# Kernel optimization log

Measured on AMD Instinct MI355X. Metric: run time of the kernel, lower is better.

Reference implementation:

```python
import jax, jax.numpy as jnp
import numpy as np

N, K, M, DIN, DOUT = 4096, 16, 65536, 256, 256


def setup_inputs() -> dict:
    key = jax.random.key(0)
    ks = jax.random.split(key, 16)
    s = 1.0 / np.sqrt(DOUT)
    x = jax.random.normal(ks[0], (N, DIN), jnp.float32)
    h_tensor = jax.random.normal(ks[1], (M, DOUT), jnp.float32)
    c_tensor = jax.random.normal(ks[2], (M, DOUT), jnp.float32)
    # variable-length child lists: lengths in [1, K], -1 padding like get_nums()
    lengths = jax.random.randint(ks[3], (N,), 1, K + 1)
    idx = jax.random.randint(ks[4], (N, K), 0, M)
    t = jnp.arange(K)[None, :]
    indice = jnp.where(t < lengths[:, None], idx, -1).astype(jnp.int32)
    W_w = jax.random.normal(ks[5], (4 * DOUT, DIN), jnp.float32) * s
    W_b = jax.random.normal(ks[6], (4 * DOUT,), jnp.float32) * s
    h0 = jax.random.normal(ks[7], (4, DOUT), jnp.float32)
    c0 = jax.random.normal(ks[8], (4, DOUT), jnp.float32)
    Wih = jax.random.normal(ks[9], (4, 2, 4 * DOUT, DOUT), jnp.float32) * s
    Whh = jax.random.normal(ks[10], (4, 2, 4 * DOUT, DOUT), jnp.float32) * s
    bih = jax.random.normal(ks[11], (4, 2, 4 * DOUT), jnp.float32) * s
    bhh = jax.random.normal(ks[12], (4, 2, 4 * DOUT), jnp.float32) * s
    fc = jax.random.normal(ks[13], (4, DOUT, 2 * DOUT), jnp.float32) * s
    return dict(x=x, h_tensor=h_tensor, c_tensor=c_tensor, indice=indice,
                W_w=W_w, W_b=W_b, h0=h0, c0=c0, Wih=Wih, Whh=Whh,
                bih=bih, bhh=bhh, fc=fc)


def _lstm_dir(xseq, mask, h_init, c_init, W_ih, W_hh, b, reverse):
    """Masked LSTM over child axis. xseq [N,K,d], mask [N,K] bool. Mimics
    pack_padded_sequence: state frozen and output 0 at padded steps."""
    d = h_init.shape[-1]
    xs = jnp.swapaxes(xseq, 0, 1)   # [K,N,d]
    ms = jnp.swapaxes(mask, 0, 1)   # [K,N]

    def step(carry, inp):
        h, c = carry
        xt, mt = inp
        g = xt @ W_ih.T + h @ W_hh.T + b        # [N,4d], gate order i,f,g,o
        i = jax.nn.sigmoid(g[:, :d])
        f = jax.nn.sigmoid(g[:, d:2 * d])
        u = jnp.tanh(g[:, 2 * d:3 * d])
        o = jax.nn.sigmoid(g[:, 3 * d:])
        c_new = f * c + i * u
        h_new = o * jnp.tanh(c_new)
        m = mt[:, None]
        return (jnp.where(m, h_new, h), jnp.where(m, c_new, c)), jnp.where(m, h_new, 0.0)

    _, ys = jax.lax.scan(step, (h_init, c_init), (xs, ms), reverse=reverse)
    return jnp.swapaxes(ys, 0, 1)   # [N,K,d]


def _bilstm_seq(xseq, mask, h0j, c0j, Wihj, Whhj, bihj, bhhj, fcj):
    n = xseq.shape[0]
    h_init = jnp.broadcast_to(h0j, (n, h0j.shape[-1]))
    c_init = jnp.broadcast_to(c0j, (n, c0j.shape[-1]))
    yf = _lstm_dir(xseq, mask, h_init, c_init, Wihj[0], Whhj[0], bihj[0] + bhhj[0], False)
    yb = _lstm_dir(xseq, mask, h_init, c_init, Wihj[1], Whhj[1], bihj[1] + bhhj[1], True)
    y = jnp.concatenate([yf, yb], axis=-1)      # [N,K,2d]
    return jnp.einsum('nkh,dh->nkd', y, fcj)    # fc (no bias); 0 stays 0 at pads


def reference(x, h_tensor, c_tensor, indice, W_w, W_b, h0, c0, Wih, Whh, bih, bhh, fc):
    mask = indice != -1                           # [N,K]
    length = mask.sum(axis=1)                     # [N], >= 1
    safe_idx = jnp.where(mask, indice, 0)
    h = h_tensor[safe_idx]                        # [N,K,d] gather of child states
    c = c_tensor[safe_idx]
    Wx = x @ W_w.T + W_b                          # [N,4d]
    d = DOUT
    Wf, Wi, Wu, Wo = Wx[:, :d], Wx[:, d:2 * d], Wx[:, 2 * d:3 * d], Wx[:, 3 * d:]
    ys = [_bilstm_seq(h, mask, h0[j], c0[j], Wih[j], Whh[j], bih[j], bhh[j], fc[j])
          for j in range(4)]                      # U_f, U_i, U_u, U_o
    # forget branch: per-child gate, masked sum over children
    branch_f_k = jax.nn.sigmoid(Wf[:, None, :] + ys[0])
    branch_f = jnp.sum(branch_f_k * c * mask[..., None], axis=1)
    # i/u/o use last valid timestep (packed LSTM y_last)
    ar = jnp.arange(x.shape[0])
    last = length - 1
    branch_i = jax.nn.sigmoid(ys[1][ar, last] + Wi)
    branch_u = jnp.tanh(ys[2][ar, last] + Wu)
    branch_o = jax.nn.sigmoid(ys[3][ar, last] + Wo)
    new_c = branch_i * branch_u + branch_f
    new_h = branch_o * jnp.tanh(new_c)
    return new_h, new_c
```

## Files before the change

kernel.cpp:

```cpp
#include <hip/hip_runtime.h>
#include <math.h>

#define N_SEQ 4096
#define KCH   16
#define DM    256
#define G4    1024
#define LP    40
#define EP    68

typedef __attribute__((ext_vector_type(8))) short bf8;
typedef __attribute__((ext_vector_type(4))) float f4;

__device__ __forceinline__ float fast_rcp(float x) { return __builtin_amdgcn_rcpf(x); }
__device__ __forceinline__ float sigf(float x)   { return fast_rcp(1.f + __expf(-x)); }
__device__ __forceinline__ float tanh_f(float x) { return 1.f - 2.f * fast_rcp(1.f + __expf(2.f * x)); }

__device__ __forceinline__ float bf2f(unsigned short u) {
    return __uint_as_float(((unsigned)u) << 16);
}
__device__ __forceinline__ unsigned short f2bf(float f) {
    unsigned u = __float_as_uint(f);
    unsigned r = (u + 0x7fffu + ((u >> 16) & 1u)) >> 16;
    return (unsigned short)r;
}
__device__ __forceinline__ unsigned pack2(float a, float b) {
    return (unsigned)f2bf(a) | ((unsigned)f2bf(b) << 16);
}

#define GLDS(gp, lp) __builtin_amdgcn_global_load_lds( \
    (const __attribute__((address_space(1))) void*)(gp), \
    (__attribute__((address_space(3))) void*)(lp), 16, 0, 0)

#define VW(n) asm volatile("s_waitcnt vmcnt(" #n ")" ::: "memory")

template<int NSEG, int LDB>
__device__ __forceinline__ void pass_pipe(
    const unsigned short* const (&segA)[NSEG],
    const unsigned short* const (&segB)[NSEG],
    unsigned short* SM,
    f4 (&acc)[4][4], int wave, int wm, int wn, int jq, int fr)
{
    constexpr int NS = NSEG * 8;
    constexpr int L  = 4;
    constexpr int NP = (NS < L) ? NS : L;

#pragma unroll
    for (int p = 0; p < NP; ++p) {
        const unsigned short* A_ = segA[p >> 3] + (p & 7) * 32;
        const unsigned short* B_ = segB[p >> 3] + (p & 7) * 32;
        unsigned short* a = SM + (p % 5) * 8192 + wave * 1024;
        unsigned short* b = a + 4096;
        GLDS(A_, a);        GLDS(A_ + 16 * DM, a + 512);
        GLDS(B_, b);        GLDS(B_ + 16 * LDB, b + 512);
    }
#pragma unroll
    for (int t = 0; t < NS; ++t) {
        const int rem = NS - 1 - t;
        if (rem >= 3)      VW(12);
        else if (rem == 2) VW(8);
        else if (rem == 1) VW(4);
        else               VW(0);
        __builtin_amdgcn_s_barrier();

        if (t + L < NS) {
            const int tn = t + L;
            const unsigned short* A_ = segA[tn >> 3] + (tn & 7) * 32;
            const unsigned short* B_ = segB[tn >> 3] + (tn & 7) * 32;
            unsigned short* a = SM + (tn % 5) * 8192 + wave * 1024;
            unsigned short* b = a + 4096;
            GLDS(A_, a);    GLDS(A_ + 16 * DM, a + 512);
            GLDS(B_, b);    GLDS(B_ + 16 * LDB, b + 512);
        }

        const unsigned short* Ab = SM + (t % 5) * 8192;
        const unsigned short* Bb = Ab + 4096;
        bf8 af[4], bb[4];
#pragma unroll
        for (int i = 0; i < 4; ++i)
            af[i] = *(const bf8*)(Ab + (wm + i * 16 + fr) * 32 + jq);
#pragma unroll
        for (int j = 0; j < 4; ++j)
            bb[j] = *(const bf8*)(Bb + (wn + j * 16 + fr) * 32 + jq);

        __builtin_amdgcn_s_setprio(1);
#pragma unroll
        for (int i = 0; i < 4; ++i)
#pragma unroll
            for (int j = 0; j < 4; ++j)
                acc[i][j] = __builtin_amdgcn_mfma_f32_16x16x32_bf16(
                    af[i], bb[j], acc[i][j], 0, 0, 0);
        __builtin_amdgcn_s_setprio(0);
    }
}

template<int KLEN>
__device__ __forceinline__ void pass_bf(
    const unsigned short* __restrict__ aRow,
    const unsigned short* __restrict__ bRow,
    unsigned short* Asm, unsigned short* Bsm, f4 (&acc)[4][4])
{
    const int tid  = threadIdx.x;
    const int kh   = (tid & 1) * 16;
    const int srow = tid >> 1;
    const int lane = tid & 63, wave = tid >> 6;
    const int wm = (wave >> 1) * 64, wn = (wave & 1) * 64;
    const int fr = lane & 15, fk = (lane >> 4) * 8;
    unsigned short* da = Asm + srow * LP + kh;
    unsigned short* db = Bsm + srow * LP + kh;

    for (int k0 = 0; k0 < KLEN; k0 += 32) {
        __syncthreads();
        *(int4*)(da)     = *(const int4*)(aRow + k0 + kh);
        *(int4*)(da + 8) = *(const int4*)(aRow + k0 + kh + 8);
        *(int4*)(db)     = *(const int4*)(bRow + k0 + kh);
        *(int4*)(db + 8) = *(const int4*)(bRow + k0 + kh + 8);
        __syncthreads();
        bf8 af[4], bb[4];
#pragma unroll
        for (int i = 0; i < 4; ++i)
            af[i] = *(const bf8*)(Asm + (wm + i * 16 + fr) * LP + fk);
#pragma unroll
        for (int j = 0; j < 4; ++j)
            bb[j] = *(const bf8*)(Bsm + (wn + j * 16 + fr) * LP + fk);
#pragma unroll
        for (int i = 0; i < 4; ++i)
#pragma unroll
            for (int j = 0; j < 4; ++j)
                acc[i][j] = __builtin_amdgcn_mfma_f32_16x16x32_bf16(
                    af[i], bb[j], acc[i][j], 0, 0, 0);
    }
}

template<int KLEN>
__device__ __forceinline__ void pass_f32(
    const float* __restrict__ aRow,
    const unsigned short* __restrict__ bRow,
    unsigned short* Asm, unsigned short* Bsm, f4 (&acc)[4][4])
{
    const int tid  = threadIdx.x;
    const int kh   = (tid & 1) * 16;
    const int srow = tid >> 1;
    const int lane = tid & 63, wave = tid >> 6;
    const int wm = (wave >> 1) * 64, wn = (wave & 1) * 64;
    const int fr = lane & 15, fk = (lane >> 4) * 8;
    unsigned short* da = Asm + srow * LP + kh;
    unsigned short* db = Bsm + srow * LP + kh;

    for (int k0 = 0; k0 < KLEN; k0 += 32) {
        __syncthreads();
        {
            const float* s = aRow + k0 + kh;
            float4 v0 = *(const float4*)(s);
            float4 v1 = *(const float4*)(s + 4);
            float4 v2 = *(const float4*)(s + 8);
            float4 v3 = *(const float4*)(s + 12);
            *(int4*)(da)     = make_int4(pack2(v0.x, v0.y), pack2(v0.z, v0.w),
                                         pack2(v1.x, v1.y), pack2(v1.z, v1.w));
            *(int4*)(da + 8) = make_int4(pack2(v2.x, v2.y), pack2(v2.z, v2.w),
                                         pack2(v3.x, v3.y), pack2(v3.z, v3.w));
        }
        *(int4*)(db)     = *(const int4*)(bRow + k0 + kh);
        *(int4*)(db + 8) = *(const int4*)(bRow + k0 + kh + 8);
        __syncthreads();
        bf8 af[4], bb[4];
#pragma unroll
        for (int i = 0; i < 4; ++i)
            af[i] = *(const bf8*)(Asm + (wm + i * 16 + fr) * LP + fk);
#pragma unroll
        for (int j = 0; j < 4; ++j)
            bb[j] = *(const bf8*)(Bsm + (wn + j * 16 + fr) * LP + fk);
#pragma unroll
        for (int i = 0; i < 4; ++i)
#pragma unroll
            for (int j = 0; j < 4; ++j)
                acc[i][j] = __builtin_amdgcn_mfma_f32_16x16x32_bf16(
                    af[i], bb[j], acc[i][j], 0, 0, 0);
    }
}


__global__ __launch_bounds__(256) void k_lastidx(
    const int* __restrict__ indice, int* __restrict__ last_idx)
{
    const int n = blockIdx.x * 256 + threadIdx.x;
    if (n >= N_SEQ) return;
    int len = 0;
#pragma unroll
    for (int k = 0; k < KCH; ++k) len += (indice[n * KCH + k] != -1);
    last_idx[n] = indice[n * KCH + (len - 1)];
}

__global__ __launch_bounds__(1024) void k_hh0_bsum2(
    const float* __restrict__ bih, const float* __restrict__ bhh,
    const float* __restrict__ h0, const float* __restrict__ Whh,
    float* __restrict__ bsum2)
{
    const int jz = blockIdx.x, j = jz + 1;
    const int g = threadIdx.x;
    const int jd = j * 2 + 1;
    const float* wrow = Whh + ((size_t)jd * G4 + g) * DM;
    float s = bih[jd * G4 + g] + bhh[jd * G4 + g];
    for (int h = 0; h < DM; ++h) s = fmaf(h0[j * DM + h], wrow[h], s);
    const int c = (g & 255) * 4 + (g >> 8);
    bsum2[jz * G4 + c] = s;
}

__global__ __launch_bounds__(256) void k_init_states(
    const float* __restrict__ h0, const float* __restrict__ c0,
    unsigned short* __restrict__ hA, float* __restrict__ c_state)
{
    const int row = blockIdx.x;
    const int s = row >> 12;
    const int tree = (s < 4) ? s : 0;
    const int d = threadIdx.x;
    hA[(size_t)row * DM + d]      = f2bf(h0[tree * DM + d]);
    c_state[(size_t)row * DM + d] = c0[tree * DM + d];
}

__global__ __launch_bounds__(256) void k_zero4(float4* __restrict__ p)
{
    p[(size_t)blockIdx.x * 256 + threadIdx.x] = make_float4(0.f, 0.f, 0.f, 0.f);
}

__global__ __launch_bounds__(256) void k_prep_wcat(
    const float* __restrict__ Wih, const float* __restrict__ Whh,
    const float* __restrict__ bih, const float* __restrict__ bhh,
    unsigned short* __restrict__ wcat, float* __restrict__ bsumr)
{
    const int c = blockIdx.x, s = blockIdx.y;
    const int wsel = (s < 4) ? s * 2 : 1;
    const int d = c >> 2, g = c & 3;
    const size_t srcrow = ((size_t)wsel * G4 + g * DM + d) * DM;
    unsigned short* dst = wcat + ((size_t)s * G4 + c) * 512;
    const int t = threadIdx.x;
    dst[t]       = f2bf(Wih[srcrow + t]);
    dst[256 + t] = f2bf(Whh[srcrow + t]);
    if (t == 0)
        bsumr[s * G4 + c] = bih[wsel * G4 + g * DM + d] + bhh[wsel * G4 + g * DM + d];
}

__global__ __launch_bounds__(256) void k_prep_wcat2(
    const float* __restrict__ Wih, unsigned short* __restrict__ wcat2)
{
    const int c = blockIdx.x, jz = blockIdx.y, j = jz + 1;
    const int d = c >> 2, g = c & 3;
    const size_t srcrow = ((size_t)(j * 2 + 1) * G4 + g * DM + d) * DM;
    wcat2[((size_t)jz * G4 + c) * 256 + threadIdx.x] = f2bf(Wih[srcrow + threadIdx.x]);
}

__global__ __launch_bounds__(256) void k_prep_fcb(
    const float* __restrict__ fc, unsigned short* __restrict__ fcb)
{
    const int dout = blockIdx.x, z = blockIdx.y, t = threadIdx.x;
    fcb[((size_t)z * DM + dout) * DM + t] = f2bf(fc[(size_t)dout * 512 + z * DM + t]);
}

__global__ __launch_bounds__(256) void k_prep_fcb2(
    const float* __restrict__ fc, unsigned short* __restrict__ fcb2)
{
    const int dout = blockIdx.x, jz = blockIdx.y, j = jz + 1, t = threadIdx.x;
    const float* src = fc + ((size_t)j * DM + dout) * 512;
    unsigned short* dst = fcb2 + ((size_t)jz * DM + dout) * 512;
    dst[t]       = f2bf(src[t]);
    dst[t + 256] = f2bf(src[t + 256]);
}

__global__ __launch_bounds__(256) void k_prep_wwb(
    const float* __restrict__ W_w, unsigned short* __restrict__ wwb)
{
    const size_t i = (size_t)blockIdx.x * 256 + threadIdx.x;
    wwb[i] = f2bf(W_w[i]);
}

__device__ __forceinline__ void gather_slice(
    const float* __restrict__ h_tensor, const int* __restrict__ indice,
    unsigned short* __restrict__ xbuf, int zz, int kk, int blk)
{
    const int row = blk * 64 + (threadIdx.x >> 2);
    const int cb  = (threadIdx.x & 3) * 64;
    int idx = indice[row * KCH + kk]; if (idx < 0) idx = 0;
    const float* src = h_tensor + (size_t)idx * DM + cb;
    unsigned short* dst = xbuf + ((size_t)zz * N_SEQ + row) * DM + cb;
#pragma unroll
    for (int c = 0; c < 64; c += 4) {
        float4 v = *(const float4*)(src + c);
        *(uint2*)(dst + c) = make_uint2(pack2(v.x, v.y), pack2(v.z, v.w));
    }
}

__global__ __launch_bounds__(256) void k_gather_x0(
    const float* __restrict__ h_tensor, const int* __restrict__ indice,
    unsigned short* __restrict__ xbuf)
{
    const int slice = blockIdx.x >> 6, blk = blockIdx.x & 63;
    gather_slice(h_tensor, indice, xbuf, slice, slice ? (KCH - 1) : 0, blk);
}

__global__ __launch_bounds__(256) void k_scan_merged(
    const unsigned short* __restrict__ xb_cur, unsigned short* __restrict__ xb_nxt,
    const unsigned short* __restrict__ yb_prev, unsigned short* __restrict__ yb_cur,
    const int* __restrict__ indice, const float* __restrict__ h_tensor,
    const unsigned short* __restrict__ h_in, unsigned short* __restrict__ h_out,
    float* __restrict__ c_state,
    const unsigned short* __restrict__ wcat, const float* __restrict__ bsumr,
    const unsigned short* __restrict__ fcb, unsigned short* __restrict__ ys0,
    int r)
{
    __shared__ __align__(16) unsigned short SMEM[40960];

    const int tid  = threadIdx.x;
    const int lane = tid & 63, wave = tid >> 6;
    const int wm = (wave >> 1) * 64, wn = (wave & 1) * 64;
    const int fr = lane & 15;
    const int jq = ((lane >> 4) ^ ((fr >> 1) & 3)) * 8;
    const int lr = wave * 32 + (lane >> 2);
    const int jl = ((lane & 3) ^ ((lane >> 3) & 3)) * 8;

    const int bz = blockIdx.z;

    if (bz == 5) {
        const int id5 = blockIdx.x + 8 * blockIdx.y;
        if (id5 >= 128) {
            const int rr = r + 1;
            if (rr >= KCH) return;
            const int g = id5 - 128;
            const int zz = g >> 6;
            gather_slice(h_tensor, indice, xb_nxt, zz,
                         zz ? (KCH - 1 - rr) : rr, g & 63);
            return;
        }
        if (r == 0) return;
        const int rp = r - 1;
        const int z = id5 >> 6;
        const int kslice = z ? (KCH - 1 - rp) : rp;
        const int row0 = (id5 & 31) * 128;
        const int c0 = ((id5 >> 5) & 1) * 128;

        const unsigned short* ay0 = yb_prev + ((size_t)z * N_SEQ + row0 + lr) * DM + jl;
        const unsigned short* bf0 = fcb + ((size_t)z * DM + c0 + lr) * DM + jl;

        f4 acc[4][4];
#pragma unroll
        for (int i = 0; i < 4; ++i)
#pragma unroll
            for (int j = 0; j < 4; ++j) acc[i][j] = (f4)(0.f);
        {
            const unsigned short* const segA[1] = { ay0 };
            const unsigned short* const segB[1] = { bf0 };
            pass_pipe<1, 256>(segA, segB, SMEM, acc, wave, wm, wn, jq, fr);
        }

#pragma unroll
        for (int i = 0; i < 4; ++i)
#pragma unroll
            for (int j = 0; j < 4; ++j) {
                const int col = c0 + wn + j * 16 + fr;
#pragma unroll
                for (int reg = 0; reg < 4; ++reg) {
                    const int rowg = row0 + wm + i * 16 + (lane >> 4) * 4 + reg;
                    const size_t ix = ((size_t)rowg * KCH + kslice) * DM + col;
                    ys0[ix] = f2bf(bf2f(ys0[ix]) + acc[i][j][reg]);
                }
            }
        return;
    }

    const int s = bz;
    const int k = (s < 4) ? r : (KCH - 1 - r);
    const int z = (s < 4) ? 0 : 1;
    const int bn = blockIdx.y & 7;
    const int bm = (blockIdx.y >> 3) * 8 + blockIdx.x;
    const int row0 = bm * 128, c0 = bn * 128;

    const unsigned short* xz = xb_cur + (size_t)z * N_SEQ * DM;
    const unsigned short* hs_in = h_in + (size_t)s * N_SEQ * DM;
    const unsigned short* ax0 = xz + (size_t)(row0 + lr) * DM + jl;
    const unsigned short* ah0 = hs_in + (size_t)(row0 + lr) * DM + jl;
    const unsigned short* bw0 = wcat + ((size_t)s * G4 + c0 + lr) * 512 + jl;

    f4 acc[4][4];
#pragma unroll
    for (int i = 0; i < 4; ++i)
#pragma unroll
        for (int j = 0; j < 4; ++j) acc[i][j] = (f4)(0.f);

    {
        const unsigned short* const segA[2] = { ax0, ah0 };
        const unsigned short* const segB[2] = { bw0, bw0 + 256 };
        pass_pipe<2, 512>(segA, segB, SMEM, acc, wave, wm, wn, jq, fr);
    }

    float* sc = (float*)SMEM + wave * (16 * EP);
    __syncthreads();
    const int kprev = (s < 4) ? (k - 1) : (k + 1);
#pragma unroll
    for (int i = 0; i < 4; ++i) {
#pragma unroll
        for (int j = 0; j < 4; ++j) {
            const int colL = j * 16 + fr;
            const int rbase = (lane >> 4) * 4;
#pragma unroll
            for (int reg = 0; reg < 4; ++reg)
                sc[(rbase + reg) * EP + colL] = acc[i][j][reg];
        }
        asm volatile("s_waitcnt lgkmcnt(0)" ::: "memory");
        __builtin_amdgcn_sched_barrier(0);
        const int rowg = row0 + wm + i * 16 + fr;
        const bool m = (indice[rowg * KCH + k] != -1);
        const bool mpv = (r == 0) ? true : (indice[rowg * KCH + kprev] != -1);
#pragma unroll
        for (int q = 0; q < 4; ++q) {
            const int dL = (lane >> 4) + q * 4;
            const f4 gv = *(const f4*)(sc + fr * EP + dL * 4);
            const f4 bb = *(const f4*)(bsumr + s * G4 + c0 + wn + dL * 4);
            const int d = ((c0 + wn) >> 2) + dL;
            const size_t cix = ((size_t)s * N_SEQ + rowg) * DM + d;
            unsigned short hv = 0;
            if (m) {
                const float ii = sigf(gv.x + bb.x);
                const float ff = sigf(gv.y + bb.y);
                const float uu = tanh_f(gv.z + bb.z);
                const float oo = sigf(gv.w + bb.w);
                const float c_old = c_state[cix];
                const float cn = ff * c_old + ii * uu;
                c_state[cix] = cn;
                hv = f2bf(oo * tanh_f(cn));
                h_out[cix] = hv;
            } else if (mpv) {
                h_out[cix] = hs_in[(size_t)rowg * DM + d];
            }
            if (s == 0)
                yb_cur[(size_t)rowg * DM + d] = m ? hv : (unsigned short)0;
            else if (s == 4)
                yb_cur[(size_t)(N_SEQ + rowg) * DM + d] = m ? hv : (unsigned short)0;
        }
        asm volatile("s_waitcnt lgkmcnt(0)" ::: "memory");
        __builtin_amdgcn_sched_barrier(0);
    }
}

__global__ __launch_bounds__(256) void k_acc_tail(
    const unsigned short* __restrict__ ybuf, const unsigned short* __restrict__ fcb,
    unsigned short* __restrict__ ys0)
{
    __shared__ __align__(16) unsigned short SMEM[40960];
    const int tid = threadIdx.x;
    const int lane = tid & 63, wave = tid >> 6;
    const int wm = (wave >> 1) * 64, wn = (wave & 1) * 64;
    const int fr = lane & 15;
    const int jq = ((lane >> 4) ^ ((fr >> 1) & 3)) * 8;
    const int lr = wave * 32 + (lane >> 2);
    const int jl = ((lane & 3) ^ ((lane >> 3) & 3)) * 8;

    const int z = blockIdx.z;
    const int kslice = z ? 0 : (KCH - 1);
    const int row0 = blockIdx.y * 128, c0 = blockIdx.x * 128;

    const unsigned short* ay0 = ybuf + ((size_t)z * N_SEQ + row0 + lr) * DM + jl;
    const unsigned short* bf0 = fcb + ((size_t)z * DM + c0 + lr) * DM + jl;

    f4 acc[4][4];
#pragma unroll
    for (int i = 0; i < 4; ++i)
#pragma unroll
        for (int j = 0; j < 4; ++j) acc[i][j] = (f4)(0.f);
    {
        const unsigned short* const segA[1] = { ay0 };
        const unsigned short* const segB[1] = { bf0 };
        pass_pipe<1, 256>(segA, segB, SMEM, acc, wave, wm, wn, jq, fr);
    }

#pragma unroll
    for (int i = 0; i < 4; ++i)
#pragma unroll
        for (int j = 0; j < 4; ++j) {
            const int col = c0 + wn + j * 16 + fr;
#pragma unroll
            for (int reg = 0; reg < 4; ++reg) {
                const int rowg = row0 + wm + i * 16 + (lane >> 4) * 4 + reg;
                const size_t ix = ((size_t)rowg * KCH + kslice) * DM + col;
                ys0[ix] = f2bf(bf2f(ys0[ix]) + acc[i][j][reg]);
            }
        }
}


__global__ __launch_bounds__(256) void k_bwd_mfma(
    const float* __restrict__ h_tensor, const int* __restrict__ last_idx,
    const unsigned short* __restrict__ wcat2, const float* __restrict__ bsum2,
    const float* __restrict__ c0, unsigned short* __restrict__ yb_last)
{
    __shared__ __align__(16) unsigned short SMEM[2 * 128 * LP];
    const int jz = blockIdx.z, j = jz + 1;
    const int row0 = blockIdx.y * 128, c0t = blockIdx.x * 128;
    const int tid = threadIdx.x;
    const int srow = tid >> 1;

    const float* aF = h_tensor + (size_t)last_idx[row0 + srow] * DM;
    const unsigned short* bR = wcat2 + ((size_t)jz * G4 + c0t + srow) * 256;

    f4 acc[4][4];
#pragma unroll
    for (int i = 0; i < 4; ++i)
#pragma unroll
        for (int jj = 0; jj < 4; ++jj) acc[i][jj] = (f4)(0.f);

    pass_f32<256>(aF, bR, SMEM, SMEM + 128 * LP, acc);

    const int lane = tid & 63, wave = tid >> 6;
    const int wm = (wave >> 1) * 64, wn = (wave & 1) * 64;
    float* sc = (float*)SMEM + wave * (16 * EP);

    __syncthreads();
#pragma unroll
    for (int i = 0; i < 4; ++i) {
#pragma unroll
        for (int jj = 0; jj < 4; ++jj) {
            const int colL = jj * 16 + (lane & 15);
            const int rbase = (lane >> 4) * 4;
#pragma unroll
            for (int reg = 0; reg < 4; ++reg)
                sc[(rbase + reg) * EP + colL] = acc[i][jj][reg];
        }
        __syncthreads();
        const int rowg = row0 + wm + i * 16 + (lane & 15);
#pragma unroll
        for (int q = 0; q < 4; ++q) {
            const int dL = (lane >> 4) + q * 4;
            const f4 gv = *(const f4*)(sc + (lane & 15) * EP + dL * 4);
            const f4 bb = *(const f4*)(bsum2 + jz * G4 + c0t + wn + dL * 4);
            const int d = ((c0t + wn) >> 2) + dL;
            const float ii = sigf(gv.x + bb.x);
            const float ff = sigf(gv.y + bb.y);
            const float uu = tanh_f(gv.z + bb.z);
            const float oo = sigf(gv.w + bb.w);
            const float cn = ff * c0[j * DM + d] + ii * uu;
            yb_last[((size_t)jz * N_SEQ + rowg) * DM + d] = f2bf(oo * tanh_f(cn));
        }
        __syncthreads();
    }
}

__global__ __launch_bounds__(256) void k_wx_mfma(
    const float* __restrict__ x, const unsigned short* __restrict__ wwb,
    const float* __restrict__ W_b, unsigned short* __restrict__ Wx)
{
    __shared__ __align__(16) unsigned short SMEM[2 * 128 * LP];
    const int row0 = blockIdx.y * 128, c0 = blockIdx.x * 128;
    const int tid = threadIdx.x;
    const int srow = tid >> 1;

    const float* aF = x + (size_t)(row0 + srow) * DM;
    const unsigned short* bR = wwb + (size_t)(c0 + srow) * DM;

    f4 acc[4][4];
#pragma unroll
    for (int i = 0; i < 4; ++i)
#pragma unroll
        for (int j = 0; j < 4; ++j) acc[i][j] = (f4)(0.f);

    pass_f32<256>(aF, bR, SMEM, SMEM + 128 * LP, acc);

    const int lane = tid & 63, wave = tid >> 6;
    const int wm = (wave >> 1) * 64, wn = (wave & 1) * 64;
#pragma unroll
    for (int i = 0; i < 4; ++i)
#pragma unroll
        for (int j = 0; j < 4; ++j) {
            const int col = c0 + wn + j * 16 + (lane & 15);
            const float bv = W_b[col];
#pragma unroll
            for (int reg = 0; reg < 4; ++reg) {
                const int rowg = row0 + wm + i * 16 + (lane >> 4) * 4 + reg;
                Wx[(size_t)rowg * G4 + col] = f2bf(acc[i][j][reg] + bv);
            }
        }
}

__global__ __launch_bounds__(256) void k_fc_last_mfma(
    const unsigned short* __restrict__ h_final, const unsigned short* __restrict__ yb_last,
    const unsigned short* __restrict__ fcb2, unsigned short* __restrict__ ys_last)
{
    __shared__ __align__(16) unsigned short SMEM[2 * 128 * LP];
    const int jz = blockIdx.z;
    const int row0 = blockIdx.y * 128, c0 = blockIdx.x * 128;
    const int tid = threadIdx.x;
    const int srow = tid >> 1;

    const unsigned short* aH1 = h_final + ((size_t)(1 + jz) * N_SEQ + row0 + srow) * DM;
    const unsigned short* aH2 = yb_last + ((size_t)jz * N_SEQ + row0 + srow) * DM;
    const unsigned short* bR  = fcb2 + ((size_t)jz * DM + c0 + srow) * 512;

    f4 acc[4][4];
#pragma unroll
    for (int i = 0; i < 4; ++i)
#pragma unroll
        for (int j = 0; j < 4; ++j) acc[i][j] = (f4)(0.f);

    pass_bf<256>(aH1, bR, SMEM, SMEM + 128 * LP, acc);
    pass_bf<256>(aH2, bR + 256, SMEM, SMEM + 128 * LP, acc);

    const int lane = tid & 63, wave = tid >> 6;
    const int wm = (wave >> 1) * 64, wn = (wave & 1) * 64;
#pragma unroll
    for (int i = 0; i < 4; ++i)
#pragma unroll
        for (int j = 0; j < 4; ++j) {
            const int col = c0 + wn + j * 16 + (lane & 15);
#pragma unroll
            for (int reg = 0; reg < 4; ++reg) {
                const int rowg = row0 + wm + i * 16 + (lane >> 4) * 4 + reg;
                ys_last[((size_t)jz * N_SEQ + rowg) * DM + col] = f2bf(acc[i][j][reg]);
            }
        }
}

__global__ __launch_bounds__(256) void k_final(
    const unsigned short* __restrict__ Wx, const unsigned short* __restrict__ ys0,
    const unsigned short* __restrict__ ys_last, const float* __restrict__ c_tensor,
    const int* __restrict__ indice, float* __restrict__ out)
{
    const int n = blockIdx.x, d = threadIdx.x;
    const float Wf = bf2f(Wx[(size_t)n * G4 + d]);
    const float Wi = bf2f(Wx[(size_t)n * G4 + DM + d]);
    const float Wu = bf2f(Wx[(size_t)n * G4 + 2 * DM + d]);
    const float Wo = bf2f(Wx[(size_t)n * G4 + 3 * DM + d]);
    float bf = 0.f;
#pragma unroll
    for (int k = 0; k < KCH; ++k) {
        const int id = indice[n * KCH + k];
        if (id >= 0)
            bf += sigf(Wf + bf2f(ys0[((size_t)n * KCH + k) * DM + d])) *
                  c_tensor[(size_t)id * DM + d];
    }
    const float bi = sigf(bf2f(ys_last[((size_t)0 * N_SEQ + n) * DM + d]) + Wi);
    const float bu = tanh_f(bf2f(ys_last[((size_t)1 * N_SEQ + n) * DM + d]) + Wu);
    const float bo = sigf(bf2f(ys_last[((size_t)2 * N_SEQ + n) * DM + d]) + Wo);
    const float nc = bi * bu + bf;
    const float nh = bo * tanh_f(nc);
    out[(size_t)n * DM + d] = nh;
    out[(size_t)N_SEQ * DM + (size_t)n * DM + d] = nc;
}

extern "C" void kernel_launch(void* const* d_in, const int* in_sizes, int n_in,
                              void* d_out, int out_size, void* d_ws, size_t ws_size,
                              hipStream_t stream)
{
    const float* x        = (const float*)d_in[0];
    const float* h_tensor = (const float*)d_in[1];
    const float* c_tensor = (const float*)d_in[2];
    const int*   indice   = (const int*)d_in[3];
    const float* W_w      = (const float*)d_in[4];
    const float* W_b      = (const float*)d_in[5];
    const float* h0       = (const float*)d_in[6];
    const float* c0       = (const float*)d_in[7];
    const float* Wih      = (const float*)d_in[8];
    const float* Whh      = (const float*)d_in[9];
    const float* bih      = (const float*)d_in[10];
    const float* bhh      = (const float*)d_in[11];
    const float* fc       = (const float*)d_in[12];
    float* out = (float*)d_out;

    char* base = (char*)d_ws;
    float*          c_state  = (float*)(base + 0);
    int*            last_idx = (int*)  (base + 20971520);
    float*          bsumr    = (float*)(base + 20987904);
    unsigned short* hA       = (unsigned short*)(base + 21008384);
    unsigned short* hB       = (unsigned short*)(base + 31494144);
    unsigned short* ys0      = (unsigned short*)(base + 41979904);
    unsigned short* ybufA    = (unsigned short*)(base + 75534336);
    unsigned short* ybufB    = (unsigned short*)(base + 79728640);
    unsigned short* xbufA    = (unsigned short*)(base + 83922944);
    unsigned short* fcb      = (unsigned short*)(base + 88117248);
    unsigned short* postbuf  = (unsigned short*)(base + 88379392);
    unsigned short* wcat     = (unsigned short*)(base + 92573696);
    const size_t need = 97816576;
    if (ws_size < need) return;

    unsigned short* xbufB   = postbuf;
    unsigned short* wcat2   = postbuf;
    unsigned short* fcb2    = postbuf + 786432;
    unsigned short* wwb     = postbuf + 1179648;
    float*          bsum2   = (float*)(postbuf + 1441792);
    unsigned short* yb_last = ybufA;
    unsigned short* ys_last = hB;
    unsigned short* WxBuf   = hA;

    k_lastidx<<<16, 256, 0, stream>>>(indice, last_idx);
    k_init_states<<<5 * N_SEQ, 256, 0, stream>>>(h0, c0, hA, c_state);
    k_zero4<<<8192, 256, 0, stream>>>((float4*)ys0);
    k_prep_wcat<<<dim3(G4, 5), 256, 0, stream>>>(Wih, Whh, bih, bhh, wcat, bsumr);
    k_prep_fcb<<<dim3(DM, 2), 256, 0, stream>>>(fc, fcb);
    k_gather_x0<<<128, 256, 0, stream>>>(h_tensor, indice, xbufA);

    for (int r = 0; r < KCH; ++r) {
        const unsigned short* xb_cur = (r & 1) ? xbufB : xbufA;
        unsigned short* xb_nxt       = (r & 1) ? xbufA : xbufB;
        const unsigned short* yb_prev = (r & 1) ? ybufA : ybufB;
        unsigned short* yb_cur        = (r & 1) ? ybufB : ybufA;
        const unsigned short* h_in = (r & 1) ? hB : hA;
        unsigned short* h_out      = (r & 1) ? hA : hB;
        k_scan_merged<<<dim3(8, 32, 6), 256, 0, stream>>>(
            xb_cur, xb_nxt, yb_prev, yb_cur, indice, h_tensor,
            h_in, h_out, c_state, wcat, bsumr, fcb, ys0, r);
    }

    k_acc_tail<<<dim3(2, 32, 2), 256, 0, stream>>>(ybufB, fcb, ys0);

    k_prep_wcat2<<<dim3(G4, 3), 256, 0, stream>>>(Wih, wcat2);
    k_hh0_bsum2<<<3, 1024, 0, stream>>>(bih, bhh, h0, Whh, bsum2);
    k_prep_fcb2<<<dim3(DM, 3), 256, 0, stream>>>(fc, fcb2);
    k_prep_wwb<<<1024, 256, 0, stream>>>(W_w, wwb);

    k_bwd_mfma<<<dim3(8, 32, 3), 256, 0, stream>>>(
        h_tensor, last_idx, wcat2, bsum2, c0, yb_last);
    k_fc_last_mfma<<<dim3(2, 32, 3), 256, 0, stream>>>(hA, yb_last, fcb2, ys_last);
    k_wx_mfma<<<dim3(8, 32), 256, 0, stream>>>(x, wwb, W_b, WxBuf);

    k_final<<<N_SEQ, 256, 0, stream>>>(WxBuf, ys0, ys_last, c_tensor, indice, out);
}
```

Measured before the change: 1.208 ms.

## Double M-tile to 256 rows in scan and tail GEMMs, three-stage pipeline

Recurrent scan and tail GEMM blocks now cover 256 rows instead of 128, so each wave holds an 8x4 accumulator tile. The aim is to raise MFMA work per B-tile load and halve the number of scan blocks. The LDS pipeline drops from five stages at depth four to three stages at depth two, and the grid is reworked: a seventh z-slice carries part of the next-step gather. In exchange, per-thread register use roughly doubles, which may cut occupancy, and shallower prefetch can expose more memory latency.

```diff
diff --git a/kernel.cpp b/kernel.cpp
--- a/kernel.cpp
+++ b/kernel.cpp
@@ -34,49 +34,47 @@
 #define VW(n) asm volatile("s_waitcnt vmcnt(" #n ")" ::: "memory")
 
 template<int NSEG, int LDB>
-__device__ __forceinline__ void pass_pipe(
+__device__ __forceinline__ void pass_fat(
     const unsigned short* const (&segA)[NSEG],
     const unsigned short* const (&segB)[NSEG],
     unsigned short* SM,
-    f4 (&acc)[4][4], int wave, int wm, int wn, int jq, int fr)
+    f4 (&acc)[8][4], int wave, int wm, int wn, int jq, int fr)
 {
     constexpr int NS = NSEG * 8;
-    constexpr int L  = 4;
+    constexpr int L  = 2;
     constexpr int NP = (NS < L) ? NS : L;
 
 #pragma unroll
     for (int p = 0; p < NP; ++p) {
         const unsigned short* A_ = segA[p >> 3] + (p & 7) * 32;
         const unsigned short* B_ = segB[p >> 3] + (p & 7) * 32;
-        unsigned short* a = SM + (p % 5) * 8192 + wave * 1024;
-        unsigned short* b = a + 4096;
-        GLDS(A_, a);        GLDS(A_ + 16 * DM, a + 512);
-        GLDS(B_, b);        GLDS(B_ + 16 * LDB, b + 512);
+        unsigned short* a = SM + (p % 3) * 12288 + wave * 1024;
+        unsigned short* b = SM + (p % 3) * 12288 + 8192 + wave * 1024;
+        GLDS(A_, a);                 GLDS(A_ + 16 * DM, a + 512);
+        GLDS(A_ + 128 * DM, a + 4096); GLDS(A_ + 144 * DM, a + 4608);
+        GLDS(B_, b);                 GLDS(B_ + 16 * LDB, b + 512);
     }
 #pragma unroll
     for (int t = 0; t < NS; ++t) {
-        const int rem = NS - 1 - t;
-        if (rem >= 3)      VW(12);
-        else if (rem == 2) VW(8);
-        else if (rem == 1) VW(4);
-        else               VW(0);
+        if (t < NS - 1) VW(6); else VW(0);
         __builtin_amdgcn_s_barrier();
 
         if (t + L < NS) {
             const int tn = t + L;
             const unsigned short* A_ = segA[tn >> 3] + (tn & 7) * 32;
             const unsigned short* B_ = segB[tn >> 3] + (tn & 7) * 32;
-            unsigned short* a = SM + (tn % 5) * 8192 + wave * 1024;
-            unsigned short* b = a + 4096;
-            GLDS(A_, a);    GLDS(A_ + 16 * DM, a + 512);
-            GLDS(B_, b);    GLDS(B_ + 16 * LDB, b + 512);
-        }
-
-        const unsigned short* Ab = SM + (t % 5) * 8192;
-        const unsigned short* Bb = Ab + 4096;
-        bf8 af[4], bb[4];
-#pragma unroll
-        for (int i = 0; i < 4; ++i)
+            unsigned short* a = SM + (tn % 3) * 12288 + wave * 1024;
+            unsigned short* b = SM + (tn % 3) * 12288 + 8192 + wave * 1024;
+            GLDS(A_, a);                 GLDS(A_ + 16 * DM, a + 512);
+            GLDS(A_ + 128 * DM, a + 4096); GLDS(A_ + 144 * DM, a + 4608);
+            GLDS(B_, b);                 GLDS(B_ + 16 * LDB, b + 512);
+        }
+
+        const unsigned short* Ab = SM + (t % 3) * 12288;
+        const unsigned short* Bb = Ab + 8192;
+        bf8 af[8], bb[4];
+#pragma unroll
+        for (int i = 0; i < 8; ++i)
             af[i] = *(const bf8*)(Ab + (wm + i * 16 + fr) * 32 + jq);
 #pragma unroll
         for (int j = 0; j < 4; ++j)
@@ -84,7 +82,7 @@
 
         __builtin_amdgcn_s_setprio(1);
 #pragma unroll
-        for (int i = 0; i < 4; ++i)
+        for (int i = 0; i < 8; ++i)
 #pragma unroll
             for (int j = 0; j < 4; ++j)
                 acc[i][j] = __builtin_amdgcn_mfma_f32_16x16x32_bf16(
@@ -296,7 +294,7 @@
     gather_slice(h_tensor, indice, xbuf, slice, slice ? (KCH - 1) : 0, blk);
 }
 
-__global__ __launch_bounds__(256) void k_scan_merged(
+__global__ __launch_bounds__(256, 2) void k_scan_merged(
     const unsigned short* __restrict__ xb_cur, unsigned short* __restrict__ xb_nxt,
     const unsigned short* __restrict__ yb_prev, unsigned short* __restrict__ yb_cur,
     const int* __restrict__ indice, const float* __restrict__ h_tensor,
@@ -306,11 +304,11 @@
     const unsigned short* __restrict__ fcb, unsigned short* __restrict__ ys0,
     int r)
 {
-    __shared__ __align__(16) unsigned short SMEM[40960];
+    __shared__ __align__(16) unsigned short SMEM[36864];
 
     const int tid  = threadIdx.x;
     const int lane = tid & 63, wave = tid >> 6;
-    const int wm = (wave >> 1) * 64, wn = (wave & 1) * 64;
+    const int wm = (wave >> 1) * 128, wn = (wave & 1) * 64;
     const int fr = lane & 15;
     const int jq = ((lane >> 4) ^ ((fr >> 1) & 3)) * 8;
     const int lr = wave * 32 + (lane >> 2);
@@ -318,40 +316,45 @@
 
     const int bz = blockIdx.z;
 
-    if (bz == 5) {
+    if (bz >= 5) {
         const int id5 = blockIdx.x + 8 * blockIdx.y;
-        if (id5 >= 128) {
+        if (bz == 6) {
+            if (id5 >= 64) return;
             const int rr = r + 1;
             if (rr >= KCH) return;
-            const int g = id5 - 128;
-            const int zz = g >> 6;
-            gather_slice(h_tensor, indice, xb_nxt, zz,
-                         zz ? (KCH - 1 - rr) : rr, g & 63);
+            gather_slice(h_tensor, indice, xb_nxt, 1, KCH - 1 - rr, id5);
+            return;
+        }
+        if (id5 >= 64) {
+            const int rr = r + 1;
+            if (rr >= KCH) return;
+            gather_slice(h_tensor, indice, xb_nxt, 0, rr, id5 - 64);
             return;
         }
         if (r == 0) return;
         const int rp = r - 1;
-        const int z = id5 >> 6;
+        const int z = id5 >> 5;
+        const int rem = id5 & 31;
         const int kslice = z ? (KCH - 1 - rp) : rp;
-        const int row0 = (id5 & 31) * 128;
-        const int c0 = ((id5 >> 5) & 1) * 128;
+        const int row0 = (rem >> 1) * 256;
+        const int c0 = (rem & 1) * 128;
 
         const unsigned short* ay0 = yb_prev + ((size_t)z * N_SEQ + row0 + lr) * DM + jl;
         const unsigned short* bf0 = fcb + ((size_t)z * DM + c0 + lr) * DM + jl;
 
-        f4 acc[4][4];
-#pragma unroll
-        for (int i = 0; i < 4; ++i)
+        f4 acc[8][4];
+#pragma unroll
+        for (int i = 0; i < 8; ++i)
 #pragma unroll
             for (int j = 0; j < 4; ++j) acc[i][j] = (f4)(0.f);
         {
             const unsigned short* const segA[1] = { ay0 };
             const unsigned short* const segB[1] = { bf0 };
-            pass_pipe<1, 256>(segA, segB, SMEM, acc, wave, wm, wn, jq, fr);
-        }
-
-#pragma unroll
-        for (int i = 0; i < 4; ++i)
+            pass_fat<1, 256>(segA, segB, SMEM, acc, wave, wm, wn, jq, fr);
+        }
+
+#pragma unroll
+        for (int i = 0; i < 8; ++i)
 #pragma unroll
             for (int j = 0; j < 4; ++j) {
                 const int col = c0 + wn + j * 16 + fr;
@@ -370,7 +373,7 @@
     const int z = (s < 4) ? 0 : 1;
     const int bn = blockIdx.y & 7;
     const int bm = (blockIdx.y >> 3) * 8 + blockIdx.x;
-    const int row0 = bm * 128, c0 = bn * 128;
+    const int row0 = bm * 256, c0 = bn * 128;
 
     const unsigned short* xz = xb_cur + (size_t)z * N_SEQ * DM;
     const unsigned short* hs_in = h_in + (size_t)s * N_SEQ * DM;
@@ -378,23 +381,23 @@
     const unsigned short* ah0 = hs_in + (size_t)(row0 + lr) * DM + jl;
     const unsigned short* bw0 = wcat + ((size_t)s * G4 + c0 + lr) * 512 + jl;
 
-    f4 acc[4][4];
-#pragma unroll
-    for (int i = 0; i < 4; ++i)
+    f4 acc[8][4];
+#pragma unroll
+    for (int i = 0; i < 8; ++i)
 #pragma unroll
         for (int j = 0; j < 4; ++j) acc[i][j] = (f4)(0.f);
 
     {
         const unsigned short* const segA[2] = { ax0, ah0 };
         const unsigned short* const segB[2] = { bw0, bw0 + 256 };
-        pass_pipe<2, 512>(segA, segB, SMEM, acc, wave, wm, wn, jq, fr);
+        pass_fat<2, 512>(segA, segB, SMEM, acc, wave, wm, wn, jq, fr);
     }
 
     float* sc = (float*)SMEM + wave * (16 * EP);
     __syncthreads();
     const int kprev = (s < 4) ? (k - 1) : (k + 1);
 #pragma unroll
-    for (int i = 0; i < 4; ++i) {
+    for (int i = 0; i < 8; ++i) {
 #pragma unroll
         for (int j = 0; j < 4; ++j) {
             const int colL = j * 16 + fr;
@@ -439,14 +442,14 @@
     }
 }
 
-__global__ __launch_bounds__(256) void k_acc_tail(
+__global__ __launch_bounds__(256, 2) void k_acc_tail(
     const unsigned short* __restrict__ ybuf, const unsigned short* __restrict__ fcb,
     unsigned short* __restrict__ ys0)
 {
-    __shared__ __align__(16) unsigned short SMEM[40960];
+    __shared__ __align__(16) unsigned short SMEM[36864];
     const int tid = threadIdx.x;
     const int lane = tid & 63, wave = tid >> 6;
-    const int wm = (wave >> 1) * 64, wn = (wave & 1) * 64;
+    const int wm = (wave >> 1) * 128, wn = (wave & 1) * 64;
     const int fr = lane & 15;
     const int jq = ((lane >> 4) ^ ((fr >> 1) & 3)) * 8;
     const int lr = wave * 32 + (lane >> 2);
@@ -454,24 +457,24 @@
 
     const int z = blockIdx.z;
     const int kslice = z ? 0 : (KCH - 1);
-    const int row0 = blockIdx.y * 128, c0 = blockIdx.x * 128;
+    const int row0 = blockIdx.y * 256, c0 = blockIdx.x * 128;
 
     const unsigned short* ay0 = ybuf + ((size_t)z * N_SEQ + row0 + lr) * DM + jl;
     const unsigned short* bf0 = fcb + ((size_t)z * DM + c0 + lr) * DM + jl;
 
-    f4 acc[4][4];
-#pragma unroll
-    for (int i = 0; i < 4; ++i)
+    f4 acc[8][4];
+#pragma unroll
+    for (int i = 0; i < 8; ++i)
 #pragma unroll
         for (int j = 0; j < 4; ++j) acc[i][j] = (f4)(0.f);
     {
         const unsigned short* const segA[1] = { ay0 };
         const unsigned short* const segB[1] = { bf0 };
-        pass_pipe<1, 256>(segA, segB, SMEM, acc, wave, wm, wn, jq, fr);
-    }
-
-#pragma unroll
-    for (int i = 0; i < 4; ++i)
+        pass_fat<1, 256>(segA, segB, SMEM, acc, wave, wm, wn, jq, fr);
+    }
+
+#pragma unroll
+    for (int i = 0; i < 8; ++i)
 #pragma unroll
         for (int j = 0; j < 4; ++j) {
             const int col = c0 + wn + j * 16 + fr;
@@ -700,12 +703,12 @@
         unsigned short* yb_cur        = (r & 1) ? ybufB : ybufA;
         const unsigned short* h_in = (r & 1) ? hB : hA;
         unsigned short* h_out      = (r & 1) ? hA : hB;
-        k_scan_merged<<<dim3(8, 32, 6), 256, 0, stream>>>(
+        k_scan_merged<<<dim3(8, 16, 7), 256, 0, stream>>>(
             xb_cur, xb_nxt, yb_prev, yb_cur, indice, h_tensor,
             h_in, h_out, c_state, wcat, bsumr, fcb, ys0, r);
     }
 
-    k_acc_tail<<<dim3(2, 32, 2), 256, 0, stream>>>(ybufB, fcb, ys0);
+    k_acc_tail<<<dim3(2, 16, 2), 256, 0, stream>>>(ybufB, fcb, ys0);
 
     k_prep_wcat2<<<dim3(G4, 3), 256, 0, stream>>>(Wih, wcat2);
     k_hh0_bsum2<<<3, 1024, 0, stream>>>(bih, bhh, h0, Whh, bsum2);
```

New measurement: 1.316 ms. +9.0%, slower.
